# Optimization experiments

Measured on AMD Instinct MI355X. Metric: run time of the kernel, lower is better.

The kernel has to match this reference:

```python
import jax, jax.numpy as jnp
import numpy as np

N_HEADS = 16
DIM = 1024
HEAD_DIM = DIM // N_HEADS

def setup_inputs() -> dict:
    key = jax.random.key(0)
    ks = jax.random.split(key, 5)
    B, S = 4, 2048
    x = jax.random.normal(ks[0], (B, S, DIM), dtype=jnp.float32)
    # PyTorch Linear-style params (stored as [in, out] for x @ W)
    sc = 1.0 / np.sqrt(DIM)
    W_qkv = jax.random.uniform(ks[1], (DIM, 3 * DIM), jnp.float32, -sc, sc)
    b_qkv = jax.random.uniform(ks[2], (3 * DIM,), jnp.float32, -sc, sc)
    W_o = jax.random.uniform(ks[3], (DIM, DIM), jnp.float32, -sc, sc)
    b_o = jax.random.uniform(ks[4], (DIM,), jnp.float32, -sc, sc)
    return {"x": x, "W_qkv": W_qkv, "b_qkv": b_qkv, "W_o": W_o, "b_o": b_o}

def reference(x, W_qkv, b_qkv, W_o, b_o):
    B, S, D = x.shape
    qkv = x @ W_qkv + b_qkv                       # [B,S,3D]
    q, k, v = jnp.split(qkv, 3, axis=2)
    # [B,S,D] -> [B,H,S,hd]
    q = q.reshape(B, S, N_HEADS, HEAD_DIM).transpose(0, 2, 1, 3)
    k = k.reshape(B, S, N_HEADS, HEAD_DIM).transpose(0, 2, 1, 3)
    v = v.reshape(B, S, N_HEADS, HEAD_DIM).transpose(0, 2, 1, 3)
    aff = jnp.einsum('bhqd,bhkd->bhqk', q, k) / jnp.sqrt(jnp.float32(HEAD_DIM))
    causal = jnp.tril(jnp.ones((S, S), dtype=bool))  # [S,S]
    aff = jnp.where(causal[None, None], aff, jnp.float32(-jnp.inf))
    attn = jax.nn.softmax(aff, axis=3)
    # dropout p=0.0 (eval): identity
    out = jnp.einsum('bhqk,bhkd->bhqd', attn, v)
    out = out.transpose(0, 2, 1, 3).reshape(B, S, D)
    return out @ W_o + b_o
```

## Files before the change

### kernel.cpp

```cpp
#include <hip/hip_runtime.h>

typedef unsigned short u16;
typedef short bf16x8 __attribute__((ext_vector_type(8)));
typedef float f32x4 __attribute__((ext_vector_type(4)));
typedef unsigned short ushort8v __attribute__((ext_vector_type(8)));
typedef unsigned short us4 __attribute__((ext_vector_type(4)));
typedef float f4v __attribute__((ext_vector_type(4)));

#define LOG2E 1.4426950408889634f
#define FIXMAX_C (12.0f * LOG2E)

static __device__ __forceinline__ float bf2f(u16 h) {
    unsigned int u = ((unsigned int)h) << 16;
    return __builtin_bit_cast(float, u);
}
static __device__ __forceinline__ u16 f2bf(float f) {
    unsigned int u = __builtin_bit_cast(unsigned int, f);
    u += 0x7FFFu + ((u >> 16) & 1u);
    return (u16)(u >> 16);
}
static __device__ __forceinline__ void ld_lds16(const u16* g, u16* l) {
    __builtin_amdgcn_global_load_lds((const __attribute__((address_space(1))) void*)g,
                                     (__attribute__((address_space(3))) void*)l, 16, 0, 0);
}
#define MFMA16(a, b, c) __builtin_amdgcn_mfma_f32_16x16x32_bf16(a, b, c, 0, 0, 0)
#define SW(r, g) (((r) << 6) + ((((g) ^ ((r) & 7))) << 3))

__global__ void cvt_cast(const float* __restrict__ src, u16* __restrict__ dst, int n4) {
    int i = blockIdx.x * blockDim.x + threadIdx.x;
    const int stride = gridDim.x * blockDim.x;
    for (; i < n4; i += stride) {
        f4v v = *(const f4v*)(src + (size_t)i * 4);
        us4 o;
        o[0] = f2bf(v[0]); o[1] = f2bf(v[1]); o[2] = f2bf(v[2]); o[3] = f2bf(v[3]);
        *(us4*)(dst + (size_t)i * 4) = o;
    }
}

__global__ __launch_bounds__(256) void cvt_T(const float* __restrict__ W, u16* __restrict__ WT,
                                             int N, int K) {
    __shared__ u16 tT[64][72];
    const int tid = threadIdx.x;
    const int tiles_n = N >> 6;
    const int tn = blockIdx.x % tiles_n, tk = blockIdx.x / tiles_n;
    const int rr = tid >> 4, c4 = (tid & 15) * 4;
    #pragma unroll
    for (int i = 0; i < 4; i++) {
        int kk = rr + i * 16;
        f4v v = *(const f4v*)&W[(size_t)(tk * 64 + kk) * N + tn * 64 + c4];
        #pragma unroll
        for (int j = 0; j < 4; j++) tT[c4 + j][kk] = f2bf(v[j]);
    }
    __syncthreads();
    const int nrow = tid >> 2, kc = (tid & 3) * 16;
    ushort8v a = *(const ushort8v*)&tT[nrow][kc];
    ushort8v b = *(const ushort8v*)&tT[nrow][kc + 8];
    u16* dst = WT + (size_t)(tn * 64 + nrow) * K + tk * 64 + kc;
    *(ushort8v*)dst = a;
    *(ushort8v*)(dst + 8) = b;
}

template <int MODE>
__global__ __launch_bounds__(256) void gemm128(
        const u16* __restrict__ A, const u16* __restrict__ BT,
        const u16* __restrict__ bias, void* __restrict__ Cout,
        u16* __restrict__ vT, int K, int nx) {
    __shared__ u16 As[2][128][32];
    __shared__ u16 Bs[2][128][32];
    const int tid = threadIdx.x, lane = tid & 63, wid = tid >> 6;
    const int lm = lane & 15, q = lane >> 4;
    const int id = blockIdx.x;
    const int panel = id / (nx * 8), rem = id % (nx * 8);
    const int bx = rem >> 3, by = panel * 8 + (rem & 7);
    const int m0 = by * 128, n0 = bx * 128;
    const int wm = (wid >> 1) * 64, wn = (wid & 1) * 64;
    const int w32 = wid * 32;
    f32x4 acc[4][4] = {};

    const u16* gA = A + (size_t)(m0 + w32 + (lane >> 2)) * K + (lane & 3) * 8;
    const u16* gB = BT + (size_t)(n0 + w32 + (lane >> 2)) * K + (lane & 3) * 8;

    for (int kb = 0; kb < K; kb += 64) {
        __syncthreads();
        #pragma unroll
        for (int h = 0; h < 2; h++)
            #pragma unroll
            for (int i = 0; i < 2; i++) {
                ld_lds16(gA + kb + h * 32 + (size_t)i * 16 * K, &As[h][w32 + i * 16][0]);
                ld_lds16(gB + kb + h * 32 + (size_t)i * 16 * K, &Bs[h][w32 + i * 16][0]);
            }
        __syncthreads();
        #pragma unroll
        for (int kk = 0; kk < 2; kk++) {
            bf16x8 af[4], bfr[4];
            #pragma unroll
            for (int mi = 0; mi < 4; mi++) af[mi] = *(const bf16x8*)&As[kk][wm + mi * 16 + lm][q * 8];
            #pragma unroll
            for (int ni = 0; ni < 4; ni++) bfr[ni] = *(const bf16x8*)&Bs[kk][wn + ni * 16 + lm][q * 8];
            #pragma unroll
            for (int mi = 0; mi < 4; mi++)
                #pragma unroll
                for (int ni = 0; ni < 4; ni++)
                    acc[mi][ni] = MFMA16(af[mi], bfr[ni], acc[mi][ni]);
        }
    }

    if constexpr (MODE == 0) {
        u16* qkout = (u16*)Cout;
        if (n0 < 2048) {
            #pragma unroll
            for (int ni = 0; ni < 4; ni++) {
                int col = n0 + wn + ni * 16 + lm;
                float bsv = bf2f(bias[col]);
                float sc = (col < 1024) ? 0.125f : 1.0f;
                #pragma unroll
                for (int mi = 0; mi < 4; mi++)
                    #pragma unroll
                    for (int r = 0; r < 4; r++) {
                        int row = m0 + wm + mi * 16 + q * 4 + r;
                        qkout[(size_t)row * 2048 + col] = f2bf((acc[mi][ni][r] + bsv) * sc);
                    }
            }
        } else {
            const int b_ = m0 >> 11;
            const int sb = (m0 & 2047) + wm;
            #pragma unroll
            for (int ni = 0; ni < 4; ni++) {
                int col = n0 + wn + ni * 16 + lm;
                int hh = (col - 2048) >> 6, dd = (col - 2048) & 63;
                float bsv = bf2f(bias[col]);
                u16* dst = vT + ((size_t)((b_ * 16 + hh) * 64 + dd)) * 2048;
                #pragma unroll
                for (int mi = 0; mi < 4; mi++) {
                    us4 pk;
                    #pragma unroll
                    for (int r = 0; r < 4; r++) pk[r] = f2bf(acc[mi][ni][r] + bsv);
                    *(us4*)&dst[sb + mi * 16 + q * 4] = pk;
                }
            }
        }
    } else {
        float* out = (float*)Cout;
        #pragma unroll
        for (int ni = 0; ni < 4; ni++) {
            int col = n0 + wn + ni * 16 + lm;
            float bsv = bf2f(bias[col]);
            #pragma unroll
            for (int mi = 0; mi < 4; mi++)
                #pragma unroll
                for (int r = 0; r < 4; r++) {
                    int row = m0 + wm + mi * 16 + q * 4 + r;
                    out[(size_t)row * 1024 + col] = acc[mi][ni][r] + bsv;
                }
        }
    }
}

template <bool DIAG>
__device__ __forceinline__ void proc_tile(
        const bf16x8* qf, const u16* __restrict__ ksv, const u16* __restrict__ vsv,
        u16* __restrict__ psw, f32x4* o, f32x4& lacc, const bf16x8 ones,
        int lm, int q, int m0w) {
    f32x4 s[4] = {};
    #pragma unroll
    for (int g2 = 0; g2 < 2; g2++) {
        bf16x8 a = qf[g2];
        #pragma unroll
        for (int nt = 0; nt < 4; nt++) {
            bf16x8 bb = *(const bf16x8*)&ksv[SW(nt * 16 + lm, q + 4 * g2)];
            s[nt] = MFMA16(a, bb, s[nt]);
        }
    }
    #pragma unroll
    for (int nt = 0; nt < 4; nt++)
        #pragma unroll
        for (int r = 0; r < 4; r++) {
            float v = s[nt][r];
            if constexpr (DIAG) {
                if (nt * 16 + lm > m0w + q * 4 + r) v = -3e30f;
            }
            float pv = __builtin_amdgcn_exp2f(v * LOG2E - FIXMAX_C);
            psw[SW(q * 4 + r, 2 * nt + (lm >> 3)) + (lm & 7)] = f2bf(pv);
        }
    #pragma unroll
    for (int g2 = 0; g2 < 2; g2++) {
        bf16x8 ap = *(const bf16x8*)&psw[SW(lm, q + 4 * g2)];
        lacc = MFMA16(ap, ones, lacc);
        #pragma unroll
        for (int nt = 0; nt < 4; nt++) {
            bf16x8 bv = *(const bf16x8*)&vsv[SW(nt * 16 + lm, q + 4 * g2)];
            o[nt] = MFMA16(ap, bv, o[nt]);
        }
    }
}

__global__ __launch_bounds__(256, 2) void attn3(
        const u16* __restrict__ qk, const u16* __restrict__ vT, u16* __restrict__ aw) {
    __shared__ u16 smem[16384];
    u16* ks = smem;
    u16* vs = smem + 4096;
    const int tid = threadIdx.x, lane = tid & 63, wid = tid >> 6;
    const int lm = lane & 15, q = lane >> 4;
    const int bh = blockIdx.x, p = blockIdx.y;
    const int b = bh >> 4, h = bh & 15;
    const int t[4] = {p, 15 - p, 16 + p, 31 - p};
    const size_t rowbase = (size_t)b * 2048;
    const int lr = tid >> 2, lcg = (tid & 3) * 2, lc = (tid & 3) * 16;
    const int m0w = wid * 16;
    u16* psw = smem + 8192 + wid * 1024;

    bf16x8 ones;
    #pragma unroll
    for (int j = 0; j < 8; j++) ones[j] = (short)0x3F80;

    #pragma unroll
    for (int i = 0; i < 4; i++) {
        const u16* qa = qk + (rowbase + t[i] * 64 + lr) * 2048 + h * 64 + lc;
        *(ushort8v*)&smem[i * 4096 + SW(lr, lcg)]     = *(const ushort8v*)qa;
        *(ushort8v*)&smem[i * 4096 + SW(lr, lcg + 1)] = *(const ushort8v*)(qa + 8);
    }
    __syncthreads();
    bf16x8 qf[4][2];
    #pragma unroll
    for (int i = 0; i < 4; i++)
        #pragma unroll
        for (int g2 = 0; g2 < 2; g2++)
            qf[i][g2] = *(const bf16x8*)&smem[i * 4096 + SW(m0w + lm, q + 4 * g2)];

    f32x4 o[4][4] = {};
    f32x4 lacc[4] = {};

    const u16* kg = qk + (rowbase + lr) * 2048 + 1024 + h * 64 + lc;
    const u16* vg = vT + ((size_t)bh * 64 + lr) * 2048 + lc;
    const int jmax = t[3];

    ushort8v k0 = *(const ushort8v*)kg, k1 = *(const ushort8v*)(kg + 8);
    ushort8v v0 = *(const ushort8v*)vg, v1 = *(const ushort8v*)(vg + 8);

    for (int jt = 0; jt <= jmax; ++jt) {
        __syncthreads();
        *(ushort8v*)&ks[SW(lr, lcg)] = k0; *(ushort8v*)&ks[SW(lr, lcg + 1)] = k1;
        *(ushort8v*)&vs[SW(lr, lcg)] = v0; *(ushort8v*)&vs[SW(lr, lcg + 1)] = v1;
        __syncthreads();
        if (jt < jmax) {
            const u16* kgj = kg + (size_t)(jt + 1) * 64 * 2048;
            const u16* vgj = vg + (jt + 1) * 64;
            k0 = *(const ushort8v*)kgj; k1 = *(const ushort8v*)(kgj + 8);
            v0 = *(const ushort8v*)vgj; v1 = *(const ushort8v*)(vgj + 8);
        }
        #pragma unroll
        for (int i = 0; i < 4; i++) {
            if (jt < t[i])
                proc_tile<false>(qf[i], ks, vs, psw, o[i], lacc[i], ones, lm, q, m0w);
            else if (jt == t[i])
                proc_tile<true>(qf[i], ks, vs, psw, o[i], lacc[i], ones, lm, q, m0w);
        }
    }

    #pragma unroll
    for (int i = 0; i < 4; i++) {
        f32x4 li;
        #pragma unroll
        for (int r = 0; r < 4; r++) li[r] = __builtin_amdgcn_rcpf(lacc[i][r]);
        #pragma unroll
        for (int nt = 0; nt < 4; nt++)
            #pragma unroll
            for (int r = 0; r < 4; r++) {
                int row = t[i] * 64 + m0w + q * 4 + r;
                int col = h * 64 + nt * 16 + lm;
                aw[(rowbase + row) * 1024 + col] = f2bf(o[i][nt][r] * li[r]);
            }
    }
}

extern "C" void kernel_launch(void* const* d_in, const int* in_sizes, int n_in,
                              void* d_out, int out_size, void* d_ws, size_t ws_size,
                              hipStream_t stream) {
    const float* x    = (const float*)d_in[0];
    const float* Wqkv = (const float*)d_in[1];
    const float* bqkv = (const float*)d_in[2];
    const float* Wo   = (const float*)d_in[3];
    const float* bo   = (const float*)d_in[4];
    float* out = (float*)d_out;

    u16* xb     = (u16*)d_ws;
    u16* WqkvT  = xb + (size_t)8192 * 1024;
    u16* bqkvb  = WqkvT + (size_t)3072 * 1024;
    u16* WoT    = bqkvb + 3072;
    u16* bob    = WoT + (size_t)1024 * 1024;
    u16* qk     = bob + 1024;
    u16* vT     = qk + (size_t)8192 * 2048;
    u16* aw     = vT + (size_t)64 * 64 * 2048;

    cvt_cast<<<2048, 256, 0, stream>>>(x, xb, 8192 * 1024 / 4);
    cvt_cast<<<3,    256, 0, stream>>>(bqkv, bqkvb, 3072 / 4);
    cvt_cast<<<1,    256, 0, stream>>>(bo, bob, 1024 / 4);
    cvt_T<<<48 * 16, 256, 0, stream>>>(Wqkv, WqkvT, 3072, 1024);
    cvt_T<<<16 * 16, 256, 0, stream>>>(Wo, WoT, 1024, 1024);

    gemm128<0><<<24 * 64, 256, 0, stream>>>(xb, WqkvT, bqkvb, qk, vT, 1024, 24);
    attn3<<<dim3(64, 8), 256, 0, stream>>>(qk, vT, aw);
    gemm128<1><<<8 * 64, 256, 0, stream>>>(aw, WoT, bob, out, nullptr, 1024, 8);
}
```

Baseline: 275.1 us.

## Split attention blocks into two balanced query tiles and truncate P to bf16

Each attention block now handles two causally balanced query tiles (p, 31-p) instead of four, and the grid doubles to 64x16. Shared memory drops and launch bounds rise to four blocks per CU, which cuts register pressure and raises occupancy. The cost is that each K/V tile is streamed twice as often across blocks. Separately, the softmax probabilities are converted to bf16 by truncation instead of round-to-nearest-even, saving a few ALU ops per element at a slight accuracy cost.

After: 306.9 us. +11.6%, slower.

```diff
diff --git a/kernel.cpp b/kernel.cpp
--- a/kernel.cpp
+++ b/kernel.cpp
@@ -18,6 +18,9 @@
     unsigned int u = __builtin_bit_cast(unsigned int, f);
     u += 0x7FFFu + ((u >> 16) & 1u);
     return (u16)(u >> 16);
+}
+static __device__ __forceinline__ u16 f2bf_t(float f) {
+    return (u16)(__builtin_bit_cast(unsigned int, f) >> 16);
 }
 static __device__ __forceinline__ void ld_lds16(const u16* g, u16* l) {
     __builtin_amdgcn_global_load_lds((const __attribute__((address_space(1))) void*)g,
@@ -180,7 +183,7 @@
                 if (nt * 16 + lm > m0w + q * 4 + r) v = -3e30f;
             }
             float pv = __builtin_amdgcn_exp2f(v * LOG2E - FIXMAX_C);
-            psw[SW(q * 4 + r, 2 * nt + (lm >> 3)) + (lm & 7)] = f2bf(pv);
+            psw[SW(q * 4 + r, 2 * nt + (lm >> 3)) + (lm & 7)] = f2bf_t(pv);
         }
     #pragma unroll
     for (int g2 = 0; g2 < 2; g2++) {
@@ -194,16 +197,16 @@
     }
 }
 
-__global__ __launch_bounds__(256, 2) void attn3(
+__global__ __launch_bounds__(256, 4) void attn4(
         const u16* __restrict__ qk, const u16* __restrict__ vT, u16* __restrict__ aw) {
-    __shared__ u16 smem[16384];
+    __shared__ u16 smem[12288];
     u16* ks = smem;
     u16* vs = smem + 4096;
     const int tid = threadIdx.x, lane = tid & 63, wid = tid >> 6;
     const int lm = lane & 15, q = lane >> 4;
     const int bh = blockIdx.x, p = blockIdx.y;
     const int b = bh >> 4, h = bh & 15;
-    const int t[4] = {p, 15 - p, 16 + p, 31 - p};
+    const int t0 = p, t1 = 31 - p;
     const size_t rowbase = (size_t)b * 2048;
     const int lr = tid >> 2, lcg = (tid & 3) * 2, lc = (tid & 3) * 16;
     const int m0w = wid * 16;
@@ -213,52 +216,55 @@
     #pragma unroll
     for (int j = 0; j < 8; j++) ones[j] = (short)0x3F80;
 
-    #pragma unroll
-    for (int i = 0; i < 4; i++) {
-        const u16* qa = qk + (rowbase + t[i] * 64 + lr) * 2048 + h * 64 + lc;
-        *(ushort8v*)&smem[i * 4096 + SW(lr, lcg)]     = *(const ushort8v*)qa;
-        *(ushort8v*)&smem[i * 4096 + SW(lr, lcg + 1)] = *(const ushort8v*)(qa + 8);
+    {
+        const u16* qa = qk + (rowbase + t0 * 64 + lr) * 2048 + h * 64 + lc;
+        const u16* qb = qk + (rowbase + t1 * 64 + lr) * 2048 + h * 64 + lc;
+        *(ushort8v*)&smem[SW(lr, lcg)]            = *(const ushort8v*)qa;
+        *(ushort8v*)&smem[SW(lr, lcg + 1)]        = *(const ushort8v*)(qa + 8);
+        *(ushort8v*)&smem[4096 + SW(lr, lcg)]     = *(const ushort8v*)qb;
+        *(ushort8v*)&smem[4096 + SW(lr, lcg + 1)] = *(const ushort8v*)(qb + 8);
     }
     __syncthreads();
-    bf16x8 qf[4][2];
-    #pragma unroll
-    for (int i = 0; i < 4; i++)
+    bf16x8 qf[2][2];
+    #pragma unroll
+    for (int i = 0; i < 2; i++)
         #pragma unroll
         for (int g2 = 0; g2 < 2; g2++)
             qf[i][g2] = *(const bf16x8*)&smem[i * 4096 + SW(m0w + lm, q + 4 * g2)];
 
-    f32x4 o[4][4] = {};
-    f32x4 lacc[4] = {};
+    f32x4 o[2][4] = {};
+    f32x4 lacc[2] = {};
 
     const u16* kg = qk + (rowbase + lr) * 2048 + 1024 + h * 64 + lc;
     const u16* vg = vT + ((size_t)bh * 64 + lr) * 2048 + lc;
-    const int jmax = t[3];
 
     ushort8v k0 = *(const ushort8v*)kg, k1 = *(const ushort8v*)(kg + 8);
     ushort8v v0 = *(const ushort8v*)vg, v1 = *(const ushort8v*)(vg + 8);
 
-    for (int jt = 0; jt <= jmax; ++jt) {
+    for (int jt = 0; jt <= t1; ++jt) {
         __syncthreads();
         *(ushort8v*)&ks[SW(lr, lcg)] = k0; *(ushort8v*)&ks[SW(lr, lcg + 1)] = k1;
         *(ushort8v*)&vs[SW(lr, lcg)] = v0; *(ushort8v*)&vs[SW(lr, lcg + 1)] = v1;
         __syncthreads();
-        if (jt < jmax) {
+        if (jt < t1) {
             const u16* kgj = kg + (size_t)(jt + 1) * 64 * 2048;
             const u16* vgj = vg + (jt + 1) * 64;
             k0 = *(const ushort8v*)kgj; k1 = *(const ushort8v*)(kgj + 8);
             v0 = *(const ushort8v*)vgj; v1 = *(const ushort8v*)(vgj + 8);
         }
-        #pragma unroll
-        for (int i = 0; i < 4; i++) {
-            if (jt < t[i])
-                proc_tile<false>(qf[i], ks, vs, psw, o[i], lacc[i], ones, lm, q, m0w);
-            else if (jt == t[i])
-                proc_tile<true>(qf[i], ks, vs, psw, o[i], lacc[i], ones, lm, q, m0w);
-        }
-    }
-
-    #pragma unroll
-    for (int i = 0; i < 4; i++) {
+        if (jt < t0)
+            proc_tile<false>(qf[0], ks, vs, psw, o[0], lacc[0], ones, lm, q, m0w);
+        else if (jt == t0)
+            proc_tile<true>(qf[0], ks, vs, psw, o[0], lacc[0], ones, lm, q, m0w);
+        if (jt < t1)
+            proc_tile<false>(qf[1], ks, vs, psw, o[1], lacc[1], ones, lm, q, m0w);
+        else
+            proc_tile<true>(qf[1], ks, vs, psw, o[1], lacc[1], ones, lm, q, m0w);
+    }
+
+    const int tt[2] = {t0, t1};
+    #pragma unroll
+    for (int i = 0; i < 2; i++) {
         f32x4 li;
         #pragma unroll
         for (int r = 0; r < 4; r++) li[r] = __builtin_amdgcn_rcpf(lacc[i][r]);
@@ -266,7 +272,7 @@
         for (int nt = 0; nt < 4; nt++)
             #pragma unroll
             for (int r = 0; r < 4; r++) {
-                int row = t[i] * 64 + m0w + q * 4 + r;
+                int row = tt[i] * 64 + m0w + q * 4 + r;
                 int col = h * 64 + nt * 16 + lm;
                 aw[(rowbase + row) * 1024 + col] = f2bf(o[i][nt][r] * li[r]);
             }
@@ -299,6 +305,6 @@
     cvt_T<<<16 * 16, 256, 0, stream>>>(Wo, WoT, 1024, 1024);
 
     gemm128<0><<<24 * 64, 256, 0, stream>>>(xb, WqkvT, bqkvb, qk, vT, 1024, 24);
-    attn3<<<dim3(64, 8), 256, 0, stream>>>(qk, vT, aw);
+    attn4<<<dim3(64, 16), 256, 0, stream>>>(qk, vT, aw);
     gemm128<1><<<8 * 64, 256, 0, stream>>>(aw, WoT, bob, out, nullptr, 1024, 8);
 }
```
